# Kernel optimization log

Hardware: AMD Instinct MI355X
Metric: run time of the kernel (lower is better)

## Reference

```python
import jax, jax.numpy as jnp
import numpy as np

N, C = 8192, 256
CQK = C // 8  # q/k projection dim = 32


def setup_inputs() -> dict:
    key = jax.random.key(0)
    k1, k2, k3, k4, k5 = jax.random.split(key, 5)
    f = jax.random.normal(k1, (N, C), dtype=jnp.float32)
    Wqk = jax.random.normal(k2, (CQK, C), dtype=jnp.float32) * (1.0 / np.sqrt(C))
    Wv = jax.random.normal(k3, (C, C), dtype=jnp.float32) * (1.0 / np.sqrt(C))
    bv = jax.random.normal(k4, (C,), dtype=jnp.float32) * 0.01
    gamma = jax.random.normal(k5, (1,), dtype=jnp.float32)
    return {"f": f, "Wqk": Wqk, "Wv": Wv, "bv": bv, "gamma": gamma}


def reference(f, Wqk, Wv, bv, gamma):
    # f: [N, C] point features. 1x1 convs over the point dim == per-point linear.
    q = f @ Wqk.T                      # [N, CQK] (q and k share weights)
    # energy[i, j] = <q_i, k_j>; q == k here, no 1/sqrt(d) scaling (faithful)
    energy = q @ q.T                   # [N, N]
    attn = jax.nn.softmax(energy, axis=-1)  # softmax over last dim (dim=-1)
    v = f @ Wv.T + bv                  # [N, C]
    # torch: bmm(x_v [1,C,N], attn [1,N,N]) -> out[c, j] = sum_i v[i, c] * attn[i, j]
    attn_out = jnp.einsum('ij,ic->jc', attn, v)  # [N, C]
    return gamma[0] * attn_out + f     # [N, C]
```

## Files before the change

### kernel.cpp

```cpp
#include <hip/hip_runtime.h>
#include <hip/hip_bf16.h>

#define NN 8192
#define CC 256
#define CQK 32
#define JS 4

using bf16x8 = __attribute__((ext_vector_type(8))) short;
using f16x8  = __attribute__((ext_vector_type(8))) _Float16;
using s16x4  = __attribute__((ext_vector_type(4))) short;
using f32x4  = __attribute__((ext_vector_type(4))) float;
using f32x16 = __attribute__((ext_vector_type(16))) float;

static __device__ __forceinline__ unsigned short f2bf(float x) {
    union { __hip_bfloat16 h; unsigned short u; } cv;
    cv.h = __float2bfloat16(x);
    return cv.u;
}
static __device__ __forceinline__ float bf2f(unsigned short u) {
    union { unsigned u; float f; } cv;
    cv.u = (unsigned)u << 16;
    return cv.f;
}
static __device__ __forceinline__ float fexp2(float x) { return __builtin_amdgcn_exp2f(x); }
static __device__ __forceinline__ int packbf(float lo, float hi) {
    union { float f; unsigned u; } a, b;
    a.f = lo; b.f = hi;
    return (int)((b.u & 0xFFFF0000u) | (a.u >> 16));
}

__global__ __launch_bounds__(256) void proj_q_kernel(
    const float* __restrict__ f, const float* __restrict__ Wqk,
    unsigned short* __restrict__ qf)
{
    __shared__ __align__(16) float fl[8][CC];
    const int t  = threadIdx.x;
    const int r0 = blockIdx.x * 8;
    {
        const float4* src = (const float4*)(f + (size_t)r0 * CC);
        float4* dst = (float4*)&fl[0][0];
        dst[t]       = src[t];
        dst[t + 256] = src[t + 256];
    }
    __syncthreads();
    const int cq = t & 31;
    const int rg = t >> 5;
    const float4* w4 = (const float4*)(Wqk + (size_t)cq * CC);
    float a = 0.f;
    for (int k4 = 0; k4 < 64; ++k4) {
        float4 wq = w4[k4];
        const float4 fv = *(const float4*)&fl[rg][k4 * 4];
        a = fmaf(wq.x, fv.x, a);
        a = fmaf(wq.y, fv.y, a);
        a = fmaf(wq.z, fv.z, a);
        a = fmaf(wq.w, fv.w, a);
    }
    a *= 1.2011224087864498f;
    union { _Float16 h; unsigned short u; } cv;
    cv.h = (_Float16)a;
    qf[(size_t)(r0 + rg) * CQK + cq] = cv.u;
}

__global__ __launch_bounds__(256, 4) void pass1v_kernel(
    const unsigned short* __restrict__ qf,
    const float* __restrict__ f, const float* __restrict__ Wv,
    const float* __restrict__ bv,
    float* __restrict__ ps, unsigned short* __restrict__ vB)
{
    __shared__ float rs[4][32];
    const int t    = threadIdx.x;
    const int lane = t & 63;
    const int w    = t >> 6;
    const int l31  = lane & 31;
    const int h    = lane >> 5;

    if (blockIdx.x < (NN / 32) * JS) {
        const int i0   = (blockIdx.x & 255) * 32;
        const int js   = blockIdx.x >> 8;
        const int JCH  = NN / JS / 4;
        const int jbase = js * (NN / JS) + w * JCH;

        const size_t qir = (size_t)(i0 + l31) * CQK;
        const f16x8 bi0 = *(const f16x8*)(qf + qir + 8 * h);
        const f16x8 bi1 = *(const f16x8*)(qf + qir + 16 + 8 * h);

        float s = 0.f;

#pragma unroll 2
        for (int st = 0; st < JCH; st += 32) {
            const size_t qjr = (size_t)(jbase + st + l31) * CQK;
            const f16x8 aj0 = *(const f16x8*)(qf + qjr + 8 * h);
            const f16x8 aj1 = *(const f16x8*)(qf + qjr + 16 + 8 * h);
            f32x16 ee = {0,0,0,0,0,0,0,0,0,0,0,0,0,0,0,0};
            ee = __builtin_amdgcn_mfma_f32_32x32x16_f16(aj0, bi0, ee, 0, 0, 0);
            ee = __builtin_amdgcn_mfma_f32_32x32x16_f16(aj1, bi1, ee, 0, 0, 0);
            float a_ = 0.f;
#pragma unroll
            for (int r = 0; r < 16; ++r) a_ += fexp2(ee[r]);
            s += a_;
        }
        s += __shfl_xor(s, 32);

        if (lane < 32) rs[w][l31] = s;
        __syncthreads();
        if (t < 32) {
            float sf = rs[0][t] + rs[1][t] + rs[2][t] + rs[3][t];
            ps[(size_t)js * NN + i0 + t] = sf;
        }
    } else {
        const int nb = (blockIdx.x - (NN / 32) * JS) * 32;
        const int cb = w * 64;

        f32x16 acc[2];
#pragma unroll
        for (int cf = 0; cf < 2; ++cf)
#pragma unroll
            for (int r = 0; r < 16; ++r) acc[cf][r] = 0.f;

        const float* frow = f + (size_t)(nb + l31) * CC;
#pragma unroll
        for (int ks = 0; ks < 16; ++ks) {
            const int k0 = ks * 16 + 8 * h;
            float4 a0 = *(const float4*)(frow + k0);
            float4 a1 = *(const float4*)(frow + k0 + 4);
            bf16x8 af;
            af[0] = (short)f2bf(a0.x); af[1] = (short)f2bf(a0.y);
            af[2] = (short)f2bf(a0.z); af[3] = (short)f2bf(a0.w);
            af[4] = (short)f2bf(a1.x); af[5] = (short)f2bf(a1.y);
            af[6] = (short)f2bf(a1.z); af[7] = (short)f2bf(a1.w);
#pragma unroll
            for (int cf = 0; cf < 2; ++cf) {
                const float* wrow = Wv + (size_t)(cb + 32 * cf + l31) * CC + k0;
                float4 b0 = *(const float4*)(wrow);
                float4 b1 = *(const float4*)(wrow + 4);
                bf16x8 bw;
                bw[0] = (short)f2bf(b0.x); bw[1] = (short)f2bf(b0.y);
                bw[2] = (short)f2bf(b0.z); bw[3] = (short)f2bf(b0.w);
                bw[4] = (short)f2bf(b1.x); bw[5] = (short)f2bf(b1.y);
                bw[6] = (short)f2bf(b1.z); bw[7] = (short)f2bf(b1.w);
                acc[cf] = __builtin_amdgcn_mfma_f32_32x32x16_bf16(af, bw, acc[cf], 0, 0, 0);
            }
        }
#pragma unroll
        for (int cf = 0; cf < 2; ++cf) {
            const int cg = cb + 32 * cf + l31;
            const float bvc = bv[cg];
#pragma unroll
            for (int rg = 0; rg < 4; ++rg) {
                const int ib = (nb >> 3) + rg;
                s16x4 pk;
#pragma unroll
                for (int r = 0; r < 4; ++r)
                    pk[r] = (short)f2bf(acc[cf][4 * rg + r] + bvc);
                *(s16x4*)(vB + ((size_t)ib * CC + cg) * 8 + 4 * h) = pk;
            }
        }
    }
}

static __device__ __forceinline__ void swap2(int a_, int b_, int& lo, int& hi) {
#if __has_builtin(__builtin_amdgcn_permlane32_swap)
    auto r = __builtin_amdgcn_permlane32_swap(a_, b_, false, false);
    lo = r[0];
    hi = r[1];
#else
    const int h_ = (threadIdx.x & 63) >> 5;
    const int pa = __shfl_xor(a_, 32);
    const int pb = __shfl_xor(b_, 32);
    lo = h_ ? pb : a_;
    hi = h_ ? b_ : pa;
#endif
}

#define LOADQF(A0, A1, NI)                                                     \
    {                                                                          \
        const size_t qnr = (size_t)((NI) + l31) * CQK;                         \
        A0 = *(const f16x8*)(qf + qnr + 8 * h);                                \
        A1 = *(const f16x8*)(qf + qnr + 16 + 8 * h);                           \
    }

#define LOADVF2(VF, I)                                                         \
    _Pragma("unroll")                                                          \
    for (int s2 = 0; s2 < 2; ++s2)                                             \
        _Pragma("unroll")                                                      \
        for (int cf = 0; cf < 4; ++cf)                                         \
            VF[s2][cf] = *(const bf16x8*)(                                     \
                vB + ((size_t)(((I) >> 3) + 2 * s2 + h) * CC + cb + 32 * cf + l31) * 8);

#define LOADB42(B4, I)                                                         \
    {                                                                          \
        const int bo_ = (I) - ibase + 4 * h;                                   \
        _Pragma("unroll")                                                      \
        for (int rg = 0; rg < 4; ++rg)                                         \
            B4[rg] = *(const f32x4*)&biasl[bo_ + 8 * rg];                      \
    }

#define ECOMPF(EE, A0, A1)                                                     \
    {                                                                          \
        f32x16 z_ = {0,0,0,0,0,0,0,0,0,0,0,0,0,0,0,0};                         \
        z_ = __builtin_amdgcn_mfma_f32_32x32x16_f16(A1, bj1, z_, 0, 0, 0);     \
        EE = __builtin_amdgcn_mfma_f32_32x32x16_f16(A0, bj0, z_, 0, 0, 0);     \
    }

#define FINISH2(EE, B4, VF)                                                    \
    {                                                                          \
        int d0[4], d1[4];                                                      \
        _Pragma("unroll")                                                      \
        for (int rg = 0; rg < 4; ++rg) {                                       \
            float p0 = fexp2(EE[4 * rg + 0] - B4[rg][0]);                      \
            float p1 = fexp2(EE[4 * rg + 1] - B4[rg][1]);                      \
            float p2 = fexp2(EE[4 * rg + 2] - B4[rg][2]);                      \
            float p3 = fexp2(EE[4 * rg + 3] - B4[rg][3]);                      \
            d0[rg] = packbf(p0, p1);                                           \
            d1[rg] = packbf(p2, p3);                                           \
        }                                                                      \
        _Pragma("unroll")                                                      \
        for (int s2 = 0; s2 < 2; ++s2) {                                       \
            union { int i[4]; bf16x8 v; } pf;                                  \
            swap2(d0[2 * s2], d0[2 * s2 + 1], pf.i[0], pf.i[2]);               \
            swap2(d1[2 * s2], d1[2 * s2 + 1], pf.i[1], pf.i[3]);               \
            _Pragma("unroll")                                                  \
            for (int cf = 0; cf < 4; ++cf)                                     \
                acc[cf] = __builtin_amdgcn_mfma_f32_32x32x16_bf16(             \
                    pf.v, VF[s2][cf], acc[cf], 0, 0, 0);                       \
        }                                                                      \
    }

template<int ISPLIT, bool DIRECT>
__global__ __launch_bounds__(256, 2) void pass2_kernel(
    const unsigned short* __restrict__ qf,
    const unsigned short* __restrict__ vB,
    const float* __restrict__ ps,
    const float* __restrict__ f,
    const float* __restrict__ gp,
    void* __restrict__ dstv)
{
    __shared__ float biasl[NN / ISPLIT];
    const int t    = threadIdx.x;
    const int lane = t & 63;
    const int w    = t >> 6;
    const int l31  = lane & 31;
    const int h    = lane >> 5;
    const int bid  = blockIdx.x;

    int jblk, isp;
    if (ISPLIT == 4) {
        isp  = (bid & 7) >> 1;
        jblk = ((bid >> 3) << 1) | (bid & 1);
    } else if (ISPLIT == 2) {
        isp  = bid & 1;
        jblk = bid >> 1;
    } else {
        isp  = 0;
        jblk = bid;
    }
    const int jb   = jblk * 64;
    const int jrow = jb + 32 * (w & 1);
    const int cb   = 128 * (w >> 1);
    const int IL   = NN / ISPLIT;
    const int ibase = isp * IL;
    const int off  = ((bid ^ (bid >> 8)) & 1) * 32;

    for (int idx = t; idx < IL; idx += 256) {
        float s = ps[ibase + idx];
#pragma unroll
        for (int k = 1; k < JS; ++k) s += ps[(size_t)k * NN + ibase + idx];
        biasl[idx] = __builtin_amdgcn_logf(s);
    }
    __syncthreads();

    const size_t qjr = (size_t)(jrow + l31) * CQK;
    const f16x8 bj0 = *(const f16x8*)(qf + qjr + 8 * h);
    const f16x8 bj1 = *(const f16x8*)(qf + qjr + 16 + 8 * h);

    f32x16 acc[4];
#pragma unroll
    for (int cf = 0; cf < 4; ++cf)
#pragma unroll
        for (int r = 0; r < 16; ++r) acc[cf][r] = 0.f;

    f32x16 eeA, eeB;
    f32x4  b4A[4], b4B[4];
    f16x8  qa0, qa1, qb0, qb1;
    bf16x8 vfA[2][4], vfB[2][4];

    const int m = IL - 1;
    const int iA0 = ibase + (off & m);
    const int iB0 = ibase + ((off + 32) & m);

    LOADQF(qa0, qa1, iA0)
    LOADB42(b4A, iA0)
    LOADVF2(vfA, iA0)
    ECOMPF(eeA, qa0, qa1)
    LOADQF(qb0, qb1, iB0)
    LOADB42(b4B, iB0)

    for (int k = 0; k < IL; k += 64) {
        const int iB = ibase + ((k + 32 + off) & m);
        const int n1 = ibase + ((k + 64 + off) & m);
        const int n2 = ibase + ((k + 96 + off) & m);
        LOADVF2(vfB, iB)
        ECOMPF(eeB, qb0, qb1)
        LOADQF(qa0, qa1, n1)
        FINISH2(eeA, b4A, vfA)
        LOADB42(b4A, n1)
        LOADVF2(vfA, n1)
        ECOMPF(eeA, qa0, qa1)
        LOADQF(qb0, qb1, n2)
        FINISH2(eeB, b4B, vfB)
        LOADB42(b4B, n2)
    }

    if (DIRECT) {
        float* dst = (float*)dstv;
        const float g = gp[0];
#pragma unroll
        for (int cf = 0; cf < 4; ++cf) {
            const int c = cb + 32 * cf + l31;
#pragma unroll
            for (int rg = 0; rg < 4; ++rg)
#pragma unroll
                for (int r = 0; r < 4; ++r) {
                    const int j = jrow + 4 * h + r + 8 * rg;
                    dst[(size_t)j * CC + c] =
                        fmaf(g, acc[cf][4 * rg + r], f[(size_t)j * CC + c]);
                }
        }
    } else {
        unsigned short* part = (unsigned short*)dstv + (size_t)isp * NN * CC;
#pragma unroll
        for (int cf = 0; cf < 4; ++cf) {
            const int c = cb + 32 * cf + l31;
#pragma unroll
            for (int rg = 0; rg < 4; ++rg)
#pragma unroll
                for (int r = 0; r < 4; ++r) {
                    const int j = jrow + 4 * h + r + 8 * rg;
                    part[(size_t)j * CC + c] = f2bf(acc[cf][4 * rg + r]);
                }
        }
    }
}

template<int SPLIT>
__global__ __launch_bounds__(256) void reduce_kernel(
    const unsigned short* __restrict__ part, const float* __restrict__ f,
    const float* __restrict__ gp, float* __restrict__ out)
{
    size_t idx = (size_t)blockIdx.x * 256 + threadIdx.x;
    float s0 = 0.f, s1 = 0.f, s2 = 0.f, s3 = 0.f;
#pragma unroll
    for (int k = 0; k < SPLIT; ++k) {
        const s16x4 v = *(const s16x4*)(part + (size_t)k * NN * CC + idx * 4);
        s0 += bf2f((unsigned short)v[0]);
        s1 += bf2f((unsigned short)v[1]);
        s2 += bf2f((unsigned short)v[2]);
        s3 += bf2f((unsigned short)v[3]);
    }
    const f32x4 fv = ((const f32x4*)f)[idx];
    const float g = gp[0];
    f32x4 o;
    o[0] = fmaf(g, s0, fv[0]);
    o[1] = fmaf(g, s1, fv[1]);
    o[2] = fmaf(g, s2, fv[2]);
    o[3] = fmaf(g, s3, fv[3]);
    ((f32x4*)out)[idx] = o;
}

extern "C" void kernel_launch(void* const* d_in, const int* in_sizes, int n_in,
                              void* d_out, int out_size, void* d_ws, size_t ws_size,
                              hipStream_t stream) {
    const float* f     = (const float*)d_in[0];
    const float* Wqk   = (const float*)d_in[1];
    const float* Wv    = (const float*)d_in[2];
    const float* bv    = (const float*)d_in[3];
    const float* gamma = (const float*)d_in[4];
    float* out = (float*)d_out;

    char* ws = (char*)d_ws;
    unsigned short* qf  = (unsigned short*)ws;
    unsigned short* vB  = (unsigned short*)(ws + (1 << 20));
    float* ps   = (float*)(ws + (5 << 20));
    unsigned short* part = (unsigned short*)(ws + (6 << 20));

    proj_q_kernel<<<dim3(NN / 8), dim3(256), 0, stream>>>(f, Wqk, qf);
    pass1v_kernel<<<dim3((NN / 32) * JS + NN / 32), dim3(256), 0, stream>>>(
        qf, f, Wv, bv, ps, vB);

    const size_t PB = (size_t)NN * CC * 2;
    const size_t B0 = (size_t)6 << 20;
    if (ws_size >= B0 + 4 * PB) {
        pass2_kernel<4, false><<<dim3(128 * 4), dim3(256), 0, stream>>>(qf, vB, ps, f, gamma, part);
        reduce_kernel<4><<<dim3(NN * CC / 1024), dim3(256), 0, stream>>>(part, f, gamma, out);
    } else if (ws_size >= B0 + 2 * PB) {
        pass2_kernel<2, false><<<dim3(128 * 2), dim3(256), 0, stream>>>(qf, vB, ps, f, gamma, part);
        reduce_kernel<2><<<dim3(NN * CC / 1024), dim3(256), 0, stream>>>(part, f, gamma, out);
    } else {
        pass2_kernel<1, true><<<dim3(128), dim3(256), 0, stream>>>(qf, vB, ps, f, gamma, out);
    }
}
```

Measured before the change: 122.6 us.

## Materialize bf16 attention matrix in pass1 and replace recompute with plain GEMM

When the workspace is large enough (26MB plus a 128MB N×N bf16 buffer), pass1 now writes the unnormalized exp2 attention tiles in MFMA-ready layout while accumulating row sums. A new scale kernel folds the softmax normalization into V, and pass2 becomes a plain P^T·V GEMM. This removes the second QK^T recompute and exp pass, at the cost of writing and then reading about 128MB of HBM traffic. The q and v projections are also moved into one combined kernel launch.

```diff
diff --git a/kernel.cpp b/kernel.cpp
--- a/kernel.cpp
+++ b/kernel.cpp
@@ -28,136 +28,6 @@
     a.f = lo; b.f = hi;
     return (int)((b.u & 0xFFFF0000u) | (a.u >> 16));
 }
-
-__global__ __launch_bounds__(256) void proj_q_kernel(
-    const float* __restrict__ f, const float* __restrict__ Wqk,
-    unsigned short* __restrict__ qf)
-{
-    __shared__ __align__(16) float fl[8][CC];
-    const int t  = threadIdx.x;
-    const int r0 = blockIdx.x * 8;
-    {
-        const float4* src = (const float4*)(f + (size_t)r0 * CC);
-        float4* dst = (float4*)&fl[0][0];
-        dst[t]       = src[t];
-        dst[t + 256] = src[t + 256];
-    }
-    __syncthreads();
-    const int cq = t & 31;
-    const int rg = t >> 5;
-    const float4* w4 = (const float4*)(Wqk + (size_t)cq * CC);
-    float a = 0.f;
-    for (int k4 = 0; k4 < 64; ++k4) {
-        float4 wq = w4[k4];
-        const float4 fv = *(const float4*)&fl[rg][k4 * 4];
-        a = fmaf(wq.x, fv.x, a);
-        a = fmaf(wq.y, fv.y, a);
-        a = fmaf(wq.z, fv.z, a);
-        a = fmaf(wq.w, fv.w, a);
-    }
-    a *= 1.2011224087864498f;
-    union { _Float16 h; unsigned short u; } cv;
-    cv.h = (_Float16)a;
-    qf[(size_t)(r0 + rg) * CQK + cq] = cv.u;
-}
-
-__global__ __launch_bounds__(256, 4) void pass1v_kernel(
-    const unsigned short* __restrict__ qf,
-    const float* __restrict__ f, const float* __restrict__ Wv,
-    const float* __restrict__ bv,
-    float* __restrict__ ps, unsigned short* __restrict__ vB)
-{
-    __shared__ float rs[4][32];
-    const int t    = threadIdx.x;
-    const int lane = t & 63;
-    const int w    = t >> 6;
-    const int l31  = lane & 31;
-    const int h    = lane >> 5;
-
-    if (blockIdx.x < (NN / 32) * JS) {
-        const int i0   = (blockIdx.x & 255) * 32;
-        const int js   = blockIdx.x >> 8;
-        const int JCH  = NN / JS / 4;
-        const int jbase = js * (NN / JS) + w * JCH;
-
-        const size_t qir = (size_t)(i0 + l31) * CQK;
-        const f16x8 bi0 = *(const f16x8*)(qf + qir + 8 * h);
-        const f16x8 bi1 = *(const f16x8*)(qf + qir + 16 + 8 * h);
-
-        float s = 0.f;
-
-#pragma unroll 2
-        for (int st = 0; st < JCH; st += 32) {
-            const size_t qjr = (size_t)(jbase + st + l31) * CQK;
-            const f16x8 aj0 = *(const f16x8*)(qf + qjr + 8 * h);
-            const f16x8 aj1 = *(const f16x8*)(qf + qjr + 16 + 8 * h);
-            f32x16 ee = {0,0,0,0,0,0,0,0,0,0,0,0,0,0,0,0};
-            ee = __builtin_amdgcn_mfma_f32_32x32x16_f16(aj0, bi0, ee, 0, 0, 0);
-            ee = __builtin_amdgcn_mfma_f32_32x32x16_f16(aj1, bi1, ee, 0, 0, 0);
-            float a_ = 0.f;
-#pragma unroll
-            for (int r = 0; r < 16; ++r) a_ += fexp2(ee[r]);
-            s += a_;
-        }
-        s += __shfl_xor(s, 32);
-
-        if (lane < 32) rs[w][l31] = s;
-        __syncthreads();
-        if (t < 32) {
-            float sf = rs[0][t] + rs[1][t] + rs[2][t] + rs[3][t];
-            ps[(size_t)js * NN + i0 + t] = sf;
-        }
-    } else {
-        const int nb = (blockIdx.x - (NN / 32) * JS) * 32;
-        const int cb = w * 64;
-
-        f32x16 acc[2];
-#pragma unroll
-        for (int cf = 0; cf < 2; ++cf)
-#pragma unroll
-            for (int r = 0; r < 16; ++r) acc[cf][r] = 0.f;
-
-        const float* frow = f + (size_t)(nb + l31) * CC;
-#pragma unroll
-        for (int ks = 0; ks < 16; ++ks) {
-            const int k0 = ks * 16 + 8 * h;
-            float4 a0 = *(const float4*)(frow + k0);
-            float4 a1 = *(const float4*)(frow + k0 + 4);
-            bf16x8 af;
-            af[0] = (short)f2bf(a0.x); af[1] = (short)f2bf(a0.y);
-            af[2] = (short)f2bf(a0.z); af[3] = (short)f2bf(a0.w);
-            af[4] = (short)f2bf(a1.x); af[5] = (short)f2bf(a1.y);
-            af[6] = (short)f2bf(a1.z); af[7] = (short)f2bf(a1.w);
-#pragma unroll
-            for (int cf = 0; cf < 2; ++cf) {
-                const float* wrow = Wv + (size_t)(cb + 32 * cf + l31) * CC + k0;
-                float4 b0 = *(const float4*)(wrow);
-                float4 b1 = *(const float4*)(wrow + 4);
-                bf16x8 bw;
-                bw[0] = (short)f2bf(b0.x); bw[1] = (short)f2bf(b0.y);
-                bw[2] = (short)f2bf(b0.z); bw[3] = (short)f2bf(b0.w);
-                bw[4] = (short)f2bf(b1.x); bw[5] = (short)f2bf(b1.y);
-                bw[6] = (short)f2bf(b1.z); bw[7] = (short)f2bf(b1.w);
-                acc[cf] = __builtin_amdgcn_mfma_f32_32x32x16_bf16(af, bw, acc[cf], 0, 0, 0);
-            }
-        }
-#pragma unroll
-        for (int cf = 0; cf < 2; ++cf) {
-            const int cg = cb + 32 * cf + l31;
-            const float bvc = bv[cg];
-#pragma unroll
-            for (int rg = 0; rg < 4; ++rg) {
-                const int ib = (nb >> 3) + rg;
-                s16x4 pk;
-#pragma unroll
-                for (int r = 0; r < 4; ++r)
-                    pk[r] = (short)f2bf(acc[cf][4 * rg + r] + bvc);
-                *(s16x4*)(vB + ((size_t)ib * CC + cg) * 8 + 4 * h) = pk;
-            }
-        }
-    }
-}
-
 static __device__ __forceinline__ void swap2(int a_, int b_, int& lo, int& hi) {
 #if __has_builtin(__builtin_amdgcn_permlane32_swap)
     auto r = __builtin_amdgcn_permlane32_swap(a_, b_, false, false);
@@ -170,6 +40,351 @@
     lo = h_ ? pb : a_;
     hi = h_ ? b_ : pa;
 #endif
+}
+static __device__ __forceinline__ size_t ptile_off(int jt, int it, int s2, int lane) {
+    return ((size_t)(jt * 256 + it)) * 1024 + (size_t)s2 * 512 + (size_t)lane * 8;
+}
+
+__global__ __launch_bounds__(256) void projqv_kernel(
+    const float* __restrict__ f, const float* __restrict__ Wqk,
+    const float* __restrict__ Wv, const float* __restrict__ bv,
+    unsigned short* __restrict__ qf, unsigned short* __restrict__ vB)
+{
+    __shared__ __align__(16) float fl[8][CC];
+    const int t = threadIdx.x;
+
+    if (blockIdx.x < 1024) {
+        const int r0 = blockIdx.x * 8;
+        {
+            const float4* src = (const float4*)(f + (size_t)r0 * CC);
+            float4* dst = (float4*)&fl[0][0];
+            dst[t]       = src[t];
+            dst[t + 256] = src[t + 256];
+        }
+        __syncthreads();
+        const int cq = t & 31;
+        const int rg = t >> 5;
+        const float4* w4 = (const float4*)(Wqk + (size_t)cq * CC);
+        float a = 0.f;
+        for (int k4 = 0; k4 < 64; ++k4) {
+            float4 wq = w4[k4];
+            const float4 fv = *(const float4*)&fl[rg][k4 * 4];
+            a = fmaf(wq.x, fv.x, a);
+            a = fmaf(wq.y, fv.y, a);
+            a = fmaf(wq.z, fv.z, a);
+            a = fmaf(wq.w, fv.w, a);
+        }
+        a *= 1.2011224087864498f;
+        union { _Float16 hh; unsigned short u; } cv;
+        cv.hh = (_Float16)a;
+        qf[(size_t)(r0 + rg) * CQK + cq] = cv.u;
+    } else {
+        const int lane = t & 63;
+        const int w    = t >> 6;
+        const int l31  = lane & 31;
+        const int h    = lane >> 5;
+        const int nb   = (blockIdx.x - 1024) * 32;
+        const int cb   = w * 64;
+
+        f32x16 acc[2];
+#pragma unroll
+        for (int cf = 0; cf < 2; ++cf)
+#pragma unroll
+            for (int r = 0; r < 16; ++r) acc[cf][r] = 0.f;
+
+        const float* frow = f + (size_t)(nb + l31) * CC;
+#pragma unroll
+        for (int ks = 0; ks < 16; ++ks) {
+            const int k0 = ks * 16 + 8 * h;
+            float4 a0 = *(const float4*)(frow + k0);
+            float4 a1 = *(const float4*)(frow + k0 + 4);
+            bf16x8 af;
+            af[0] = (short)f2bf(a0.x); af[1] = (short)f2bf(a0.y);
+            af[2] = (short)f2bf(a0.z); af[3] = (short)f2bf(a0.w);
+            af[4] = (short)f2bf(a1.x); af[5] = (short)f2bf(a1.y);
+            af[6] = (short)f2bf(a1.z); af[7] = (short)f2bf(a1.w);
+#pragma unroll
+            for (int cf = 0; cf < 2; ++cf) {
+                const float* wrow = Wv + (size_t)(cb + 32 * cf + l31) * CC + k0;
+                float4 b0 = *(const float4*)(wrow);
+                float4 b1 = *(const float4*)(wrow + 4);
+                bf16x8 bw;
+                bw[0] = (short)f2bf(b0.x); bw[1] = (short)f2bf(b0.y);
+                bw[2] = (short)f2bf(b0.z); bw[3] = (short)f2bf(b0.w);
+                bw[4] = (short)f2bf(b1.x); bw[5] = (short)f2bf(b1.y);
+                bw[6] = (short)f2bf(b1.z); bw[7] = (short)f2bf(b1.w);
+                acc[cf] = __builtin_amdgcn_mfma_f32_32x32x16_bf16(af, bw, acc[cf], 0, 0, 0);
+            }
+        }
+#pragma unroll
+        for (int cf = 0; cf < 2; ++cf) {
+            const int cg = cb + 32 * cf + l31;
+            const float bvc = bv[cg];
+#pragma unroll
+            for (int rg = 0; rg < 4; ++rg) {
+                const int ib = (nb >> 3) + rg;
+                s16x4 pk;
+#pragma unroll
+                for (int r = 0; r < 4; ++r)
+                    pk[r] = (short)f2bf(acc[cf][4 * rg + r] + bvc);
+                *(s16x4*)(vB + ((size_t)ib * CC + cg) * 8 + 4 * h) = pk;
+            }
+        }
+    }
+}
+
+
+__global__ __launch_bounds__(256, 4) void pass1P_kernel(
+    const unsigned short* __restrict__ qf,
+    unsigned short* __restrict__ Pp,
+    float* __restrict__ ps)
+{
+    __shared__ float rs[4][32];
+    const int t    = threadIdx.x;
+    const int lane = t & 63;
+    const int w    = t >> 6;
+    const int l31  = lane & 31;
+    const int h    = lane >> 5;
+    const int it   = blockIdx.x & 255;
+    const int js   = blockIdx.x >> 8;
+    const int JCH  = NN / JS / 4;
+    const int jbase = js * (NN / JS) + w * JCH;
+
+    const size_t qir = (size_t)(it * 32 + l31) * CQK;
+    const f16x8 ai0 = *(const f16x8*)(qf + qir + 8 * h);
+    const f16x8 ai1 = *(const f16x8*)(qf + qir + 16 + 8 * h);
+
+    float svec[16];
+#pragma unroll
+    for (int s = 0; s < 16; ++s) svec[s] = 0.f;
+
+#pragma unroll 2
+    for (int st = 0; st < JCH; st += 32) {
+        const int jg = jbase + st;
+        const size_t qjr = (size_t)(jg + l31) * CQK;
+        const f16x8 bj0 = *(const f16x8*)(qf + qjr + 8 * h);
+        const f16x8 bj1 = *(const f16x8*)(qf + qjr + 16 + 8 * h);
+        f32x16 z_ = {0,0,0,0,0,0,0,0,0,0,0,0,0,0,0,0};
+        z_ = __builtin_amdgcn_mfma_f32_32x32x16_f16(ai1, bj1, z_, 0, 0, 0);
+        const f32x16 ee = __builtin_amdgcn_mfma_f32_32x32x16_f16(ai0, bj0, z_, 0, 0, 0);
+
+        int d0[4], d1[4];
+#pragma unroll
+        for (int rg = 0; rg < 4; ++rg) {
+            const float p0 = fexp2(ee[4 * rg + 0]);
+            const float p1 = fexp2(ee[4 * rg + 1]);
+            const float p2 = fexp2(ee[4 * rg + 2]);
+            const float p3 = fexp2(ee[4 * rg + 3]);
+            svec[4 * rg + 0] += p0;
+            svec[4 * rg + 1] += p1;
+            svec[4 * rg + 2] += p2;
+            svec[4 * rg + 3] += p3;
+            d0[rg] = packbf(p0, p1);
+            d1[rg] = packbf(p2, p3);
+        }
+        const int jt = jg >> 5;
+#pragma unroll
+        for (int s2 = 0; s2 < 2; ++s2) {
+            union { int i[4]; bf16x8 v; } pf;
+            swap2(d0[2 * s2], d0[2 * s2 + 1], pf.i[0], pf.i[2]);
+            swap2(d1[2 * s2], d1[2 * s2 + 1], pf.i[1], pf.i[3]);
+            *(bf16x8*)(Pp + ptile_off(jt, it, s2, lane)) = pf.v;
+        }
+    }
+
+#pragma unroll
+    for (int off = 1; off < 32; off <<= 1)
+#pragma unroll
+        for (int s = 0; s < 16; ++s)
+            svec[s] += __shfl_xor(svec[s], off);
+
+    if (l31 == 0) {
+#pragma unroll
+        for (int s = 0; s < 16; ++s) {
+            const int islot = (s & 3) + 4 * h + 8 * (s >> 2);
+            rs[w][islot] = svec[s];
+        }
+    }
+    __syncthreads();
+    if (t < 32)
+        ps[(size_t)js * NN + it * 32 + t] = rs[0][t] + rs[1][t] + rs[2][t] + rs[3][t];
+}
+
+__global__ __launch_bounds__(256) void scalev_kernel(
+    const float* __restrict__ ps, const unsigned short* __restrict__ vB,
+    unsigned short* __restrict__ vBs)
+{
+    const int idx = blockIdx.x * 256 + threadIdx.x;
+    const int ib  = idx >> 8;
+    float rin[8];
+#pragma unroll
+    for (int ie = 0; ie < 8; ++ie) {
+        const int i = ib * 8 + ie;
+        float s = ps[i] + ps[NN + i] + ps[2 * NN + i] + ps[3 * NN + i];
+        rin[ie] = 1.0f / s;
+    }
+    const s16x4 v0 = *(const s16x4*)(vB + (size_t)idx * 8);
+    const s16x4 v1 = *(const s16x4*)(vB + (size_t)idx * 8 + 4);
+    s16x4 o0, o1;
+#pragma unroll
+    for (int k = 0; k < 4; ++k) {
+        o0[k] = (short)f2bf(bf2f((unsigned short)v0[k]) * rin[k]);
+        o1[k] = (short)f2bf(bf2f((unsigned short)v1[k]) * rin[4 + k]);
+    }
+    *(s16x4*)(vBs + (size_t)idx * 8)     = o0;
+    *(s16x4*)(vBs + (size_t)idx * 8 + 4) = o1;
+}
+
+#define GLOADVF(VF, I)                                                         \
+    _Pragma("unroll")                                                          \
+    for (int s2 = 0; s2 < 2; ++s2)                                             \
+        _Pragma("unroll")                                                      \
+        for (int cf = 0; cf < 4; ++cf)                                         \
+            VF[s2][cf] = *(const bf16x8*)(                                     \
+                vBs + ((size_t)(((I) >> 3) + 2 * s2 + h) * CC + cb + 32 * cf + l31) * 8);
+
+#define GLOADPA(PA, I)                                                         \
+    {                                                                          \
+        PA[0] = *(const bf16x8*)(Pp + ptile_off(jt, (I) >> 5, 0, lane));       \
+        PA[1] = *(const bf16x8*)(Pp + ptile_off(jt, (I) >> 5, 1, lane));       \
+    }
+
+#define GSTEP(PA, VF)                                                          \
+    _Pragma("unroll")                                                          \
+    for (int s2 = 0; s2 < 2; ++s2)                                             \
+        _Pragma("unroll")                                                      \
+        for (int cf = 0; cf < 4; ++cf)                                         \
+            acc[cf] = __builtin_amdgcn_mfma_f32_32x32x16_bf16(                 \
+                PA[s2], VF[s2][cf], acc[cf], 0, 0, 0);
+
+template<int ISPLIT, bool DIRECT>
+__global__ __launch_bounds__(256, 2) void gemm_kernel(
+    const unsigned short* __restrict__ Pp,
+    const unsigned short* __restrict__ vBs,
+    const float* __restrict__ f,
+    const float* __restrict__ gp,
+    void* __restrict__ dstv)
+{
+    const int t    = threadIdx.x;
+    const int lane = t & 63;
+    const int w    = t >> 6;
+    const int l31  = lane & 31;
+    const int h    = lane >> 5;
+    const int bid  = blockIdx.x;
+
+    int jblk, isp;
+    if (ISPLIT == 4) {
+        isp  = (bid & 7) >> 1;
+        jblk = ((bid >> 3) << 1) | (bid & 1);
+    } else if (ISPLIT == 2) {
+        isp  = bid & 1;
+        jblk = bid >> 1;
+    } else {
+        isp  = 0;
+        jblk = bid;
+    }
+    const int jrow = jblk * 64 + 32 * (w & 1);
+    const int jt   = jrow >> 5;
+    const int cb   = 128 * (w >> 1);
+    const int IL   = NN / ISPLIT;
+    const int ibase = isp * IL;
+    const int iend  = ibase + IL;
+
+    f32x16 acc[4];
+#pragma unroll
+    for (int cf = 0; cf < 4; ++cf)
+#pragma unroll
+        for (int r = 0; r < 16; ++r) acc[cf][r] = 0.f;
+
+    bf16x8 pAa[2], pAb[2];
+    bf16x8 vfA[2][4], vfB[2][4];
+
+    GLOADPA(pAa, ibase)
+    GLOADVF(vfA, ibase)
+    GLOADPA(pAb, ibase + 32)
+
+    for (int i0s = ibase; i0s < iend; i0s += 64) {
+        const int n1 = (i0s + 64 < iend) ? i0s + 64 : ibase;
+        const int n2 = (i0s + 96 < iend) ? i0s + 96 : ibase;
+        GLOADVF(vfB, i0s + 32)
+        GSTEP(pAa, vfA)
+        GLOADPA(pAa, n1)
+        GLOADVF(vfA, n1)
+        GSTEP(pAb, vfB)
+        GLOADPA(pAb, n2)
+    }
+
+    if (DIRECT) {
+        float* dst = (float*)dstv;
+        const float g = gp[0];
+#pragma unroll
+        for (int cf = 0; cf < 4; ++cf) {
+            const int c = cb + 32 * cf + l31;
+#pragma unroll
+            for (int rg = 0; rg < 4; ++rg)
+#pragma unroll
+                for (int r = 0; r < 4; ++r) {
+                    const int j = jrow + 4 * h + r + 8 * rg;
+                    dst[(size_t)j * CC + c] =
+                        fmaf(g, acc[cf][4 * rg + r], f[(size_t)j * CC + c]);
+                }
+        }
+    } else {
+        unsigned short* part = (unsigned short*)dstv + (size_t)isp * NN * CC;
+#pragma unroll
+        for (int cf = 0; cf < 4; ++cf) {
+            const int c = cb + 32 * cf + l31;
+#pragma unroll
+            for (int rg = 0; rg < 4; ++rg)
+#pragma unroll
+                for (int r = 0; r < 4; ++r) {
+                    const int j = jrow + 4 * h + r + 8 * rg;
+                    part[(size_t)j * CC + c] = f2bf(acc[cf][4 * rg + r]);
+                }
+        }
+    }
+}
+
+
+__global__ __launch_bounds__(256, 4) void pass1_kernel(
+    const unsigned short* __restrict__ qf, float* __restrict__ ps)
+{
+    __shared__ float rs[4][32];
+    const int t    = threadIdx.x;
+    const int lane = t & 63;
+    const int w    = t >> 6;
+    const int l31  = lane & 31;
+    const int h    = lane >> 5;
+    const int i0   = (blockIdx.x & 255) * 32;
+    const int js   = blockIdx.x >> 8;
+    const int JCH  = NN / JS / 4;
+    const int jbase = js * (NN / JS) + w * JCH;
+
+    const size_t qir = (size_t)(i0 + l31) * CQK;
+    const f16x8 bi0 = *(const f16x8*)(qf + qir + 8 * h);
+    const f16x8 bi1 = *(const f16x8*)(qf + qir + 16 + 8 * h);
+
+    float s = 0.f;
+#pragma unroll 2
+    for (int st = 0; st < JCH; st += 32) {
+        const size_t qjr = (size_t)(jbase + st + l31) * CQK;
+        const f16x8 aj0 = *(const f16x8*)(qf + qjr + 8 * h);
+        const f16x8 aj1 = *(const f16x8*)(qf + qjr + 16 + 8 * h);
+        f32x16 ee = {0,0,0,0,0,0,0,0,0,0,0,0,0,0,0,0};
+        ee = __builtin_amdgcn_mfma_f32_32x32x16_f16(aj0, bi0, ee, 0, 0, 0);
+        ee = __builtin_amdgcn_mfma_f32_32x32x16_f16(aj1, bi1, ee, 0, 0, 0);
+        float a_ = 0.f;
+#pragma unroll
+        for (int r = 0; r < 16; ++r) a_ += fexp2(ee[r]);
+        s += a_;
+    }
+    s += __shfl_xor(s, 32);
+    if (lane < 32) rs[w][l31] = s;
+    __syncthreads();
+    if (t < 32) {
+        float sf = rs[0][t] + rs[1][t] + rs[2][t] + rs[3][t];
+        ps[(size_t)js * NN + i0 + t] = sf;
+    }
 }
 
 #define LOADQF(A0, A1, NI)                                                     \
@@ -380,22 +595,35 @@
     char* ws = (char*)d_ws;
     unsigned short* qf  = (unsigned short*)ws;
     unsigned short* vB  = (unsigned short*)(ws + (1 << 20));
-    float* ps   = (float*)(ws + (5 << 20));
-    unsigned short* part = (unsigned short*)(ws + (6 << 20));
-
-    proj_q_kernel<<<dim3(NN / 8), dim3(256), 0, stream>>>(f, Wqk, qf);
-    pass1v_kernel<<<dim3((NN / 32) * JS + NN / 32), dim3(256), 0, stream>>>(
-        qf, f, Wv, bv, ps, vB);
-
-    const size_t PB = (size_t)NN * CC * 2;
-    const size_t B0 = (size_t)6 << 20;
-    if (ws_size >= B0 + 4 * PB) {
-        pass2_kernel<4, false><<<dim3(128 * 4), dim3(256), 0, stream>>>(qf, vB, ps, f, gamma, part);
+
+    const size_t need_new = ((size_t)26 << 20) + (size_t)NN * NN * 2;
+    if (ws_size >= need_new) {
+        unsigned short* vBs  = (unsigned short*)(ws + (5 << 20));
+        float* ps            = (float*)(ws + (9 << 20));
+        unsigned short* part = (unsigned short*)(ws + (10 << 20));
+        unsigned short* Pp   = (unsigned short*)(ws + (26 << 20));
+
+        projqv_kernel<<<dim3(1024 + NN / 32), dim3(256), 0, stream>>>(f, Wqk, Wv, bv, qf, vB);
+        pass1P_kernel<<<dim3(256 * JS), dim3(256), 0, stream>>>(qf, Pp, ps);
+        scalev_kernel<<<dim3(1024), dim3(256), 0, stream>>>(ps, vB, vBs);
+        gemm_kernel<4, false><<<dim3(128 * 4), dim3(256), 0, stream>>>(Pp, vBs, f, gamma, part);
         reduce_kernel<4><<<dim3(NN * CC / 1024), dim3(256), 0, stream>>>(part, f, gamma, out);
-    } else if (ws_size >= B0 + 2 * PB) {
-        pass2_kernel<2, false><<<dim3(128 * 2), dim3(256), 0, stream>>>(qf, vB, ps, f, gamma, part);
-        reduce_kernel<2><<<dim3(NN * CC / 1024), dim3(256), 0, stream>>>(part, f, gamma, out);
     } else {
-        pass2_kernel<1, true><<<dim3(128), dim3(256), 0, stream>>>(qf, vB, ps, f, gamma, out);
-    }
-}
+        float* ps            = (float*)(ws + (5 << 20));
+        unsigned short* part = (unsigned short*)(ws + (6 << 20));
+        const size_t PB = (size_t)NN * CC * 2;
+        const size_t B0 = (size_t)6 << 20;
+
+        projqv_kernel<<<dim3(1024 + NN / 32), dim3(256), 0, stream>>>(f, Wqk, Wv, bv, qf, vB);
+        pass1_kernel<<<dim3(256 * JS), dim3(256), 0, stream>>>(qf, ps);
+        if (ws_size >= B0 + 4 * PB) {
+            pass2_kernel<4, false><<<dim3(128 * 4), dim3(256), 0, stream>>>(qf, vB, ps, f, gamma, part);
+            reduce_kernel<4><<<dim3(NN * CC / 1024), dim3(256), 0, stream>>>(part, f, gamma, out);
+        } else if (ws_size >= B0 + 2 * PB) {
+            pass2_kernel<2, false><<<dim3(128 * 2), dim3(256), 0, stream>>>(qf, vB, ps, f, gamma, part);
+            reduce_kernel<2><<<dim3(NN * CC / 1024), dim3(256), 0, stream>>>(part, f, gamma, out);
+        } else {
+            pass2_kernel<1, true><<<dim3(128), dim3(256), 0, stream>>>(qf, vB, ps, f, gamma, out);
+        }
+    }
+}
```

Measured after the change: 137.5 us. 1.12x slower.
